# Kernel optimization log

Measured on AMD Instinct MI355X. Metric: run time of the kernel, lower is better.

The kernel has to match this reference:

```python
import jax, jax.numpy as jnp
import numpy as np

EPS = 1e-5
N_HEAD = 12
N_LAYER = 12
D = 768
VOCAB = 50257
SEQ = 1024


def layer_norm(x, w, b):
    m = jnp.mean(x, axis=-1, keepdims=True)
    v = jnp.mean(jnp.square(x - m), axis=-1, keepdims=True)
    return (x - m) * jax.lax.rsqrt(v + EPS) * w + b


def setup_inputs() -> dict:
    key = jax.random.key(0)
    ks = jax.random.split(key, 8)
    s = 0.02  # gpt2 init scale
    return {
        "input_ids": jax.random.randint(ks[0], (SEQ,), 0, VOCAB, dtype=jnp.int64 if jax.config.jax_enable_x64 else jnp.int32),
        "wte": jax.random.normal(ks[1], (VOCAB, D), jnp.float32) * s,
        "wpe": jax.random.normal(ks[2], (SEQ, D), jnp.float32) * s,
        "ln1_w": jnp.ones((N_LAYER, D), jnp.float32),
        "ln1_b": jnp.zeros((N_LAYER, D), jnp.float32),
        "qkv_w": jax.random.normal(ks[3], (N_LAYER, D, 3 * D), jnp.float32) * s,
        "qkv_b": jnp.zeros((N_LAYER, 3 * D), jnp.float32),
        "out_w": jax.random.normal(ks[4], (N_LAYER, D, D), jnp.float32) * s,
        "out_b": jnp.zeros((N_LAYER, D), jnp.float32),
        "ln2_w": jnp.ones((N_LAYER, D), jnp.float32),
        "ln2_b": jnp.zeros((N_LAYER, D), jnp.float32),
        "up_w": jax.random.normal(ks[5], (N_LAYER, D, 4 * D), jnp.float32) * s,
        "up_b": jnp.zeros((N_LAYER, 4 * D), jnp.float32),
        "down_w": jax.random.normal(ks[6], (N_LAYER, 4 * D, D), jnp.float32) * s,
        "down_b": jnp.zeros((N_LAYER, D), jnp.float32),
        "lnf_w": jnp.ones((D,), jnp.float32),
        "lnf_b": jnp.zeros((D,), jnp.float32),
    }


def _attention(x, qkv_w, qkv_b, out_w, out_b, causal_mask):
    S = x.shape[0]
    d = D // N_HEAD
    qkv = x @ qkv_w + qkv_b                  # [S, 3D]
    q, k, v = jnp.split(qkv, 3, axis=-1)     # each [S, D]
    q = q.reshape(S, N_HEAD, d)
    k = k.reshape(S, N_HEAD, d)
    v = v.reshape(S, N_HEAD, d)
    scores = jnp.einsum('shd,thd->hst', q, k) / np.sqrt(d).astype(np.float32)
    scores = jnp.where(causal_mask, scores, jnp.finfo(scores.dtype).min)
    p = jax.nn.softmax(scores, axis=-1)      # [H, S, S]
    o = jnp.einsum('hst,thd->shd', p, v).reshape(S, D)
    return o @ out_w + out_b


def reference(input_ids, wte, wpe, ln1_w, ln1_b, qkv_w, qkv_b, out_w, out_b,
              ln2_w, ln2_b, up_w, up_b, down_w, down_b, lnf_w, lnf_b):
    S = input_ids.shape[0]
    h0 = wte[input_ids] + wpe[jnp.arange(S)]        # [S, D]
    causal_mask = jnp.tril(jnp.ones((S, S), bool))

    layer_params = (ln1_w, ln1_b, qkv_w, qkv_b, out_w, out_b,
                    ln2_w, ln2_b, up_w, up_b, down_w, down_b)

    def step(x, p):
        l1w, l1b, qw, qb, ow, ob, l2w, l2b, uw, ub, dw, db = p
        x = x + _attention(layer_norm(x, l1w, l1b), qw, qb, ow, ob, causal_mask)
        x = x + (jax.nn.gelu(layer_norm(x, l2w, l2b) @ uw + ub, approximate=True) @ dw + db)
        return x, x

    h, ys = jax.lax.scan(step, h0, layer_params)
    layers_output = jnp.concatenate([h0[None], ys], axis=0)   # [L+1, S, D]
    return layer_norm(h, lnf_w, lnf_b), layers_output
```

## Files before the change

kernel.cpp:

```cpp
#include <hip/hip_runtime.h>

typedef __bf16 bf16_t;
typedef __bf16 bf16x8 __attribute__((ext_vector_type(8)));
typedef __bf16 bf16x4 __attribute__((ext_vector_type(4)));
typedef float f32x4 __attribute__((ext_vector_type(4)));

#define MFMA16(a, b, c) __builtin_amdgcn_mfma_f32_16x16x32_bf16(a, b, c, 0, 0, 0)

__device__ __forceinline__ f32x4 zero4() {
    f32x4 z = {0.f, 0.f, 0.f, 0.f};
    return z;
}

__device__ __forceinline__ float gelu_f(float v) {
    float u = 0.7978845608028654f * (v + 0.044715f * v * v * v);
    float e = __expf(2.0f * u);
    float th = 1.0f - 2.0f / (e + 1.0f);
    return 0.5f * v * (1.0f + th);
}

__device__ __forceinline__ void gload16(const bf16_t* g, bf16_t* l) {
    __builtin_amdgcn_global_load_lds((const __attribute__((address_space(1))) void*)g,
                                     (__attribute__((address_space(3))) void*)l, 16, 0, 0);
}

__global__ __launch_bounds__(256) void embed_kernel(const int* __restrict__ ids,
                                                    const float* __restrict__ wte,
                                                    const float* __restrict__ wpe,
                                                    float* __restrict__ x,
                                                    float* __restrict__ out0) {
    const int s = blockIdx.x;
    const int id = ids[s];
    const size_t base = (size_t)s * 768;
#pragma unroll
    for (int r = 0; r < 3; ++r) {
        int d = threadIdx.x + r * 256;
        float v = wte[(size_t)id * 768 + d] + wpe[base + d];
        x[base + d] = v;
        out0[base + d] = v;
    }
}

template <bool BF16OUT>
__global__ __launch_bounds__(256) void ln_kernel(const float* __restrict__ x,
                                                 const float* __restrict__ w,
                                                 const float* __restrict__ b,
                                                 void* __restrict__ outp) {
    const int row = blockIdx.x;
    const int t = threadIdx.x;
    const float* xr = x + (size_t)row * 768;
    float v0 = xr[t], v1 = xr[t + 256], v2 = xr[t + 512];
    float s = v0 + v1 + v2;
    float q = v0 * v0 + v1 * v1 + v2 * v2;
#pragma unroll
    for (int off = 32; off >= 1; off >>= 1) {
        s += __shfl_xor(s, off);
        q += __shfl_xor(q, off);
    }
    __shared__ float sh_s[4], sh_q[4];
    if ((t & 63) == 0) {
        sh_s[t >> 6] = s;
        sh_q[t >> 6] = q;
    }
    __syncthreads();
    s = sh_s[0] + sh_s[1] + sh_s[2] + sh_s[3];
    q = sh_q[0] + sh_q[1] + sh_q[2] + sh_q[3];
    const float mean = s * (1.0f / 768.0f);
    const float var = q * (1.0f / 768.0f) - mean * mean;
    const float rstd = rsqrtf(var + 1e-5f);
    float vv[3] = {v0, v1, v2};
#pragma unroll
    for (int r = 0; r < 3; ++r) {
        int d = t + r * 256;
        float y = (vv[r] - mean) * rstd * w[d] + b[d];
        if (BF16OUT)
            ((bf16_t*)outp)[(size_t)row * 768 + d] = (bf16_t)y;
        else
            ((float*)outp)[(size_t)row * 768 + d] = y;
    }
}

template <bool FINAL>
__global__ __launch_bounds__(256) void ln_reduce(const float* __restrict__ p0,
                                                 const float* __restrict__ p1,
                                                 const float* __restrict__ db,
                                                 float* __restrict__ x,
                                                 float* __restrict__ slice,
                                                 void* __restrict__ lnout,
                                                 const float* __restrict__ w,
                                                 const float* __restrict__ b) {
    const int row = blockIdx.x;
    const int t = threadIdx.x;
    const size_t base = (size_t)row * 768;
    float vv[3];
#pragma unroll
    for (int r = 0; r < 3; ++r) {
        int d = t + r * 256;
        float v = x[base + d] + p0[base + d] + p1[base + d] + db[d];
        vv[r] = v;
        x[base + d] = v;
        slice[base + d] = v;
    }
    float s = vv[0] + vv[1] + vv[2];
    float q = vv[0] * vv[0] + vv[1] * vv[1] + vv[2] * vv[2];
#pragma unroll
    for (int off = 32; off >= 1; off >>= 1) {
        s += __shfl_xor(s, off);
        q += __shfl_xor(q, off);
    }
    __shared__ float sh_s[4], sh_q[4];
    if ((t & 63) == 0) {
        sh_s[t >> 6] = s;
        sh_q[t >> 6] = q;
    }
    __syncthreads();
    s = sh_s[0] + sh_s[1] + sh_s[2] + sh_s[3];
    q = sh_q[0] + sh_q[1] + sh_q[2] + sh_q[3];
    const float mean = s * (1.0f / 768.0f);
    const float var = q * (1.0f / 768.0f) - mean * mean;
    const float rstd = rsqrtf(var + 1e-5f);
#pragma unroll
    for (int r = 0; r < 3; ++r) {
        int d = t + r * 256;
        float y = (vv[r] - mean) * rstd * w[d] + b[d];
        if (FINAL)
            ((float*)lnout)[base + d] = y;
        else
            ((bf16_t*)lnout)[base + d] = (bf16_t)y;
    }
}

__global__ __launch_bounds__(256) void transpose_cvt(const float* __restrict__ src0,
                                                     bf16_t* __restrict__ dst0, int K, int N) {
    const int l = blockIdx.z;
    const float* src = src0 + (size_t)l * K * N;
    bf16_t* dst = dst0 + (size_t)l * N * K;
    const int n0 = blockIdx.x * 32;
    const int k0 = blockIdx.y * 32;
    __shared__ float tile[32][36];
    const int t = threadIdx.x;
    const int r = t >> 3, c4 = (t & 7) * 4;
    const float4 v = *(const float4*)&src[(size_t)(k0 + r) * N + n0 + c4];
    tile[r][c4 + 0] = v.x;
    tile[r][c4 + 1] = v.y;
    tile[r][c4 + 2] = v.z;
    tile[r][c4 + 3] = v.w;
    __syncthreads();
    bf16x4 o;
    o[0] = (bf16_t)tile[c4 + 0][r];
    o[1] = (bf16_t)tile[c4 + 1][r];
    o[2] = (bf16_t)tile[c4 + 2][r];
    o[3] = (bf16_t)tile[c4 + 3][r];
    *(bf16x4*)&dst[(size_t)(n0 + r) * K + k0 + c4] = o;
}

template <int BM, int BN, bool GELU, bool RES>
__global__ __launch_bounds__(256) void gemm3(const bf16_t* __restrict__ A,
                                             const bf16_t* __restrict__ BT,
                                             const float* __restrict__ bias,
                                             const float* __restrict__ res,
                                             float* __restrict__ outF,
                                             bf16_t* __restrict__ outB, int N, int LDK,
                                             int KLEN) {
    constexpr int MW = BM / 32, NW = BN / 32;
    constexpr int TILE = (BM + BN) * 64;
    __shared__ __align__(16) bf16_t lds[2 * TILE];
    const int tid = threadIdx.x;
    const int lane = tid & 63, wv = tid >> 6, wm = wv >> 1, wn = wv & 1;
    const int lr = lane & 15, lg = lane >> 4;
    const int m0 = blockIdx.x * BM, n0 = blockIdx.y * BN;
    const bf16_t* Ap = A + (size_t)m0 * LDK + (size_t)blockIdx.z * KLEN;
    const bf16_t* Bp = BT + (size_t)n0 * LDK + (size_t)blockIdx.z * KLEN;

    f32x4 acc[MW][NW];
#pragma unroll
    for (int i = 0; i < MW; ++i)
#pragma unroll
        for (int j = 0; j < NW; ++j) acc[i][j] = zero4();

    const int KT = KLEN >> 6;

    auto stage = [&](int buf, int kt) {
        bf16_t* Ad = lds + buf * TILE;
        bf16_t* Bd = Ad + BM * 64;
#pragma unroll
        for (int i = 0; i < BM / 32; ++i) {
            int v = i * 256 + tid;
            int row = v >> 3, cg = v & 7;
            gload16(Ap + (size_t)row * LDK + kt * 64 + ((cg ^ (row & 7)) << 3), Ad + v * 8);
        }
#pragma unroll
        for (int i = 0; i < BN / 32; ++i) {
            int v = i * 256 + tid;
            int row = v >> 3, cg = v & 7;
            gload16(Bp + (size_t)row * LDK + kt * 64 + ((cg ^ (row & 7)) << 3), Bd + v * 8);
        }
    };

    stage(0, 0);
    int buf = 0;
    for (int kt = 0; kt < KT; ++kt) {
        __syncthreads();
        if (kt + 1 < KT) stage(buf ^ 1, kt + 1);
        const bf16_t* Ab = lds + buf * TILE;
        const bf16_t* Bb = Ab + BM * 64;
#pragma unroll
        for (int c = 0; c < 2; ++c) {
            bf16x8 af[MW], bfr[NW];
#pragma unroll
            for (int i = 0; i < MW; ++i) {
                int row = wm * (BM / 2) + i * 16 + lr;
                af[i] = *(const bf16x8*)&Ab[row * 64 + ((c * 32 + lg * 8) ^ ((row & 7) << 3))];
            }
#pragma unroll
            for (int j = 0; j < NW; ++j) {
                int row = wn * (BN / 2) + j * 16 + lr;
                bfr[j] = *(const bf16x8*)&Bb[row * 64 + ((c * 32 + lg * 8) ^ ((row & 7) << 3))];
            }
#pragma unroll
            for (int i = 0; i < MW; ++i)
#pragma unroll
                for (int j = 0; j < NW; ++j) acc[i][j] = MFMA16(af[i], bfr[j], acc[i][j]);
        }
        buf ^= 1;
    }

    float* o1 = outF ? outF + (size_t)blockIdx.z * ((size_t)1024 * N) : nullptr;
#pragma unroll
    for (int i = 0; i < MW; ++i) {
#pragma unroll
        for (int j = 0; j < NW; ++j) {
            const int col = n0 + wn * (BN / 2) + j * 16 + lr;
            const float bc = bias ? bias[col] : 0.f;
#pragma unroll
            for (int ii = 0; ii < 4; ++ii) {
                const int rrow = m0 + wm * (BM / 2) + i * 16 + lg * 4 + ii;
                float v = acc[i][j][ii] + bc;
                if (GELU) v = gelu_f(v);
                if (RES) v += res[(size_t)rrow * N + col];
                if (o1) o1[(size_t)rrow * N + col] = v;
                if (outB) outB[(size_t)rrow * N + col] = (bf16_t)v;
            }
        }
    }
}

__global__ __launch_bounds__(256) void attn_kernel(const bf16_t* __restrict__ qkv,
                                                   bf16_t* __restrict__ out) {
    const int qb = blockIdx.x;
    const int h = blockIdx.y;
    const int tid = threadIdx.x;
    const int w = tid >> 6, lane = tid & 63;
    const int lr = lane & 15, lg = lane >> 4;
    const int q0 = qb * 64;
    const int qr0 = q0 + w * 16;

    __shared__ bf16_t Ks[64][72];
    __shared__ bf16_t Vs[64][72];
    __shared__ bf16_t Ps[4][16][72];

    bf16x8 aq[2];
    {
        const size_t qoff = (size_t)(qr0 + lr) * 2304 + h * 64;
#pragma unroll
        for (int dt = 0; dt < 2; ++dt) {
            bf16x8 v = *(const bf16x8*)&qkv[qoff + dt * 32 + lg * 8];
#pragma unroll
            for (int i = 0; i < 8; ++i) v[i] = (bf16_t)((float)v[i] * 0.125f);
            aq[dt] = v;
        }
    }

    f32x4 oacc[4];
#pragma unroll
    for (int i = 0; i < 4; ++i) oacc[i] = zero4();
    float mrun[4], lrun[4];
#pragma unroll
    for (int i = 0; i < 4; ++i) {
        mrun[i] = -3.0e38f;
        lrun[i] = 0.f;
    }

    const int srow = tid >> 2, sseg = tid & 3;

    for (int kb = 0; kb <= qb; ++kb) {
        const int k0 = kb * 64;
        {
            const size_t roff = (size_t)(k0 + srow) * 2304 + h * 64 + sseg * 16;
            bf16x8 ka = *(const bf16x8*)&qkv[roff + 768];
            bf16x8 kbv = *(const bf16x8*)&qkv[roff + 768 + 8];
            bf16x8 va = *(const bf16x8*)&qkv[roff + 1536];
            bf16x8 vb = *(const bf16x8*)&qkv[roff + 1536 + 8];
            *(bf16x8*)&Ks[srow][sseg * 16] = ka;
            *(bf16x8*)&Ks[srow][sseg * 16 + 8] = kbv;
#pragma unroll
            for (int i = 0; i < 8; ++i) {
                Vs[sseg * 16 + i][srow] = va[i];
                Vs[sseg * 16 + 8 + i][srow] = vb[i];
            }
        }
        __syncthreads();

        f32x4 sacc[4];
#pragma unroll
        for (int i = 0; i < 4; ++i) sacc[i] = zero4();
#pragma unroll
        for (int kt = 0; kt < 4; ++kt)
#pragma unroll
            for (int dt = 0; dt < 2; ++dt) {
                bf16x8 bk = *(const bf16x8*)&Ks[kt * 16 + lr][dt * 32 + lg * 8];
                sacc[kt] = MFMA16(aq[dt], bk, sacc[kt]);
            }

        if (kb == qb) {
#pragma unroll
            for (int kt = 0; kt < 4; ++kt)
#pragma unroll
                for (int i = 0; i < 4; ++i)
                    if (k0 + kt * 16 + lr > qr0 + lg * 4 + i) sacc[kt][i] = -3.0e38f;
        }

#pragma unroll
        for (int i = 0; i < 4; ++i) {
            float rmax = fmaxf(fmaxf(sacc[0][i], sacc[1][i]), fmaxf(sacc[2][i], sacc[3][i]));
            rmax = fmaxf(rmax, __shfl_xor(rmax, 1));
            rmax = fmaxf(rmax, __shfl_xor(rmax, 2));
            rmax = fmaxf(rmax, __shfl_xor(rmax, 4));
            rmax = fmaxf(rmax, __shfl_xor(rmax, 8));
            const float mnew = fmaxf(mrun[i], rmax);
            const float sf = __expf(mrun[i] - mnew);
            mrun[i] = mnew;
            float rsum = 0.f;
#pragma unroll
            for (int kt = 0; kt < 4; ++kt) {
                float p = __expf(sacc[kt][i] - mnew);
                rsum += p;
                Ps[w][lg * 4 + i][kt * 16 + lr] = (bf16_t)p;
            }
            rsum += __shfl_xor(rsum, 1);
            rsum += __shfl_xor(rsum, 2);
            rsum += __shfl_xor(rsum, 4);
            rsum += __shfl_xor(rsum, 8);
            lrun[i] = lrun[i] * sf + rsum;
#pragma unroll
            for (int ot = 0; ot < 4; ++ot) oacc[ot][i] *= sf;
        }

        bf16x8 pa0 = *(const bf16x8*)&Ps[w][lr][lg * 8];
        bf16x8 pa1 = *(const bf16x8*)&Ps[w][lr][32 + lg * 8];
#pragma unroll
        for (int ot = 0; ot < 4; ++ot) {
            bf16x8 bv0 = *(const bf16x8*)&Vs[ot * 16 + lr][lg * 8];
            bf16x8 bv1 = *(const bf16x8*)&Vs[ot * 16 + lr][32 + lg * 8];
            oacc[ot] = MFMA16(pa0, bv0, oacc[ot]);
            oacc[ot] = MFMA16(pa1, bv1, oacc[ot]);
        }
        __syncthreads();
    }

#pragma unroll
    for (int ot = 0; ot < 4; ++ot)
#pragma unroll
        for (int i = 0; i < 4; ++i) {
            const int row = qr0 + lg * 4 + i;
            const float v = oacc[ot][i] / lrun[i];
            out[(size_t)row * 768 + h * 64 + ot * 16 + lr] = (bf16_t)v;
        }
}

extern "C" void kernel_launch(void* const* d_in, const int* in_sizes, int n_in, void* d_out,
                              int out_size, void* d_ws, size_t ws_size, hipStream_t stream) {
    const int* ids = (const int*)d_in[0];
    const float* wte = (const float*)d_in[1];
    const float* wpe = (const float*)d_in[2];
    const float* ln1_w = (const float*)d_in[3];
    const float* ln1_b = (const float*)d_in[4];
    const float* qkv_w = (const float*)d_in[5];
    const float* qkv_b = (const float*)d_in[6];
    const float* out_w = (const float*)d_in[7];
    const float* out_b = (const float*)d_in[8];
    const float* ln2_w = (const float*)d_in[9];
    const float* ln2_b = (const float*)d_in[10];
    const float* up_w = (const float*)d_in[11];
    const float* up_b = (const float*)d_in[12];
    const float* down_w = (const float*)d_in[13];
    const float* down_b = (const float*)d_in[14];
    const float* lnf_w = (const float*)d_in[15];
    const float* lnf_b = (const float*)d_in[16];

    char* ws = (char*)d_ws;
    float* x = (float*)(ws + 0);
    bf16_t* a_bf = (bf16_t*)(ws + 3145728);
    bf16_t* qkv_bf = (bf16_t*)(ws + 4718592);
    bf16_t* attn_bf = (bf16_t*)(ws + 9437184);
    bf16_t* u_bf = (bf16_t*)(ws + 11010048);
    float* p0 = (float*)(ws + 4718592);
    float* p1 = (float*)(ws + 7864320);
    bf16_t* wqkv_t = (bf16_t*)(ws + 17301504);
    bf16_t* wout_t = (bf16_t*)(ws + 59768832);
    bf16_t* wup_t = (bf16_t*)(ws + 73924608);
    bf16_t* wdown_t = (bf16_t*)(ws + 130547712);

    float* outF = (float*)d_out;
    const size_t SD = (size_t)1024 * 768;
    float* out_layers = outF + SD;

    transpose_cvt<<<dim3(72, 24, 12), 256, 0, stream>>>(qkv_w, wqkv_t, 768, 2304);
    transpose_cvt<<<dim3(24, 24, 12), 256, 0, stream>>>(out_w, wout_t, 768, 768);
    transpose_cvt<<<dim3(96, 24, 12), 256, 0, stream>>>(up_w, wup_t, 768, 3072);
    transpose_cvt<<<dim3(24, 96, 12), 256, 0, stream>>>(down_w, wdown_t, 3072, 768);

    embed_kernel<<<1024, 256, 0, stream>>>(ids, wte, wpe, x, out_layers);

    for (int l = 0; l < 12; ++l) {
        const size_t l768 = (size_t)l * 768;
        if (l == 0)
            ln_kernel<true><<<1024, 256, 0, stream>>>(x, ln1_w, ln1_b, a_bf);
        else
            ln_reduce<false><<<1024, 256, 0, stream>>>(p0, p1, down_b + (l - 1) * 768, x,
                                                       out_layers + (size_t)l * SD, a_bf,
                                                       ln1_w + l768, ln1_b + l768);
        gemm3<64, 64, false, false><<<dim3(16, 36), 256, 0, stream>>>(
            a_bf, wqkv_t + (size_t)l * 2304 * 768, qkv_b + (size_t)l * 2304, nullptr, nullptr,
            qkv_bf, 2304, 768, 768);
        attn_kernel<<<dim3(16, 12), 256, 0, stream>>>(qkv_bf, attn_bf);
        gemm3<32, 64, false, true><<<dim3(32, 12), 256, 0, stream>>>(
            attn_bf, wout_t + (size_t)l * 768 * 768, out_b + l768, x, x, nullptr, 768, 768,
            768);
        ln_kernel<true><<<1024, 256, 0, stream>>>(x, ln2_w + l768, ln2_b + l768, a_bf);
        gemm3<64, 64, true, false><<<dim3(16, 48), 256, 0, stream>>>(
            a_bf, wup_t + (size_t)l * 3072 * 768, up_b + (size_t)l * 3072, nullptr, nullptr,
            u_bf, 3072, 768, 768);
        gemm3<32, 64, false, false><<<dim3(32, 12, 2), 256, 0, stream>>>(
            u_bf, wdown_t + (size_t)l * 768 * 3072, nullptr, nullptr, p0, nullptr, 768, 3072,
            1536);
    }
    ln_reduce<true><<<1024, 256, 0, stream>>>(p0, p1, down_b + 11 * 768, x,
                                              out_layers + 12 * SD, outF, lnf_w, lnf_b);
}
```

Baseline: 1.199 ms.

## Rewrite attention with 16-row query blocks, split-K waves, and pre-transposed V

The QKV GEMM epilogue now also writes a transposed copy of V into a scratch buffer that is later reused by the MLP. The new attention kernel runs 16-query blocks over 768 workgroups of two waves, scheduled longest-first. Each wave handles alternate key blocks, reads K and V straight from global memory with no LDS staging or block barriers, and keeps P in registers. The two waves' partial softmax states are merged through LDS at the end. GEMM K-tile counts also become compile-time template constants so the loop can be fully unrolled.

```diff
diff --git a/kernel.cpp b/kernel.cpp
--- a/kernel.cpp
+++ b/kernel.cpp
@@ -4,6 +4,7 @@
 typedef __bf16 bf16x8 __attribute__((ext_vector_type(8)));
 typedef __bf16 bf16x4 __attribute__((ext_vector_type(4)));
 typedef float f32x4 __attribute__((ext_vector_type(4)));
+typedef int i32x4 __attribute__((ext_vector_type(4)));
 
 #define MFMA16(a, b, c) __builtin_amdgcn_mfma_f32_16x16x32_bf16(a, b, c, 0, 0, 0)
 
@@ -22,6 +23,12 @@
 __device__ __forceinline__ void gload16(const bf16_t* g, bf16_t* l) {
     __builtin_amdgcn_global_load_lds((const __attribute__((address_space(1))) void*)g,
                                      (__attribute__((address_space(3))) void*)l, 16, 0, 0);
+}
+
+__device__ __forceinline__ unsigned pack2(float a, float b) {
+    unsigned short ua = __builtin_bit_cast(unsigned short, (bf16_t)a);
+    unsigned short ub = __builtin_bit_cast(unsigned short, (bf16_t)b);
+    return (unsigned)ua | ((unsigned)ub << 16);
 }
 
 __global__ __launch_bounds__(256) void embed_kernel(const int* __restrict__ ids,
@@ -154,14 +161,14 @@
     *(bf16x4*)&dst[(size_t)(n0 + r) * K + k0 + c4] = o;
 }
 
-template <int BM, int BN, bool GELU, bool RES>
+template <int BM, int BN, int KTILES, bool GELU, bool RES, bool VT>
 __global__ __launch_bounds__(256) void gemm3(const bf16_t* __restrict__ A,
                                              const bf16_t* __restrict__ BT,
                                              const float* __restrict__ bias,
                                              const float* __restrict__ res,
                                              float* __restrict__ outF,
-                                             bf16_t* __restrict__ outB, int N, int LDK,
-                                             int KLEN) {
+                                             bf16_t* __restrict__ outB,
+                                             bf16_t* __restrict__ vt, int N, int LDK) {
     constexpr int MW = BM / 32, NW = BN / 32;
     constexpr int TILE = (BM + BN) * 64;
     __shared__ __align__(16) bf16_t lds[2 * TILE];
@@ -169,16 +176,14 @@
     const int lane = tid & 63, wv = tid >> 6, wm = wv >> 1, wn = wv & 1;
     const int lr = lane & 15, lg = lane >> 4;
     const int m0 = blockIdx.x * BM, n0 = blockIdx.y * BN;
-    const bf16_t* Ap = A + (size_t)m0 * LDK + (size_t)blockIdx.z * KLEN;
-    const bf16_t* Bp = BT + (size_t)n0 * LDK + (size_t)blockIdx.z * KLEN;
+    const bf16_t* Ap = A + (size_t)m0 * LDK + (size_t)blockIdx.z * (KTILES * 64);
+    const bf16_t* Bp = BT + (size_t)n0 * LDK + (size_t)blockIdx.z * (KTILES * 64);
 
     f32x4 acc[MW][NW];
 #pragma unroll
     for (int i = 0; i < MW; ++i)
 #pragma unroll
         for (int j = 0; j < NW; ++j) acc[i][j] = zero4();
-
-    const int KT = KLEN >> 6;
 
     auto stage = [&](int buf, int kt) {
         bf16_t* Ad = lds + buf * TILE;
@@ -199,9 +204,10 @@
 
     stage(0, 0);
     int buf = 0;
-    for (int kt = 0; kt < KT; ++kt) {
+#pragma unroll
+    for (int kt = 0; kt < KTILES; ++kt) {
         __syncthreads();
-        if (kt + 1 < KT) stage(buf ^ 1, kt + 1);
+        if (kt + 1 < KTILES) stage(buf ^ 1, kt + 1);
         const bf16_t* Ab = lds + buf * TILE;
         const bf16_t* Bb = Ab + BM * 64;
 #pragma unroll
@@ -232,6 +238,7 @@
         for (int j = 0; j < NW; ++j) {
             const int col = n0 + wn * (BN / 2) + j * 16 + lr;
             const float bc = bias ? bias[col] : 0.f;
+            float vr[4];
 #pragma unroll
             for (int ii = 0; ii < 4; ++ii) {
                 const int rrow = m0 + wm * (BM / 2) + i * 16 + lg * 4 + ii;
@@ -240,67 +247,52 @@
                 if (RES) v += res[(size_t)rrow * N + col];
                 if (o1) o1[(size_t)rrow * N + col] = v;
                 if (outB) outB[(size_t)rrow * N + col] = (bf16_t)v;
-            }
-        }
-    }
-}
-
-__global__ __launch_bounds__(256) void attn_kernel(const bf16_t* __restrict__ qkv,
-                                                   bf16_t* __restrict__ out) {
-    const int qb = blockIdx.x;
+                vr[ii] = v;
+            }
+            if (VT && col >= 1536) {
+                const int rrow0 = m0 + wm * (BM / 2) + i * 16 + lg * 4;
+                bf16x4 o;
+#pragma unroll
+                for (int ii = 0; ii < 4; ++ii) o[ii] = (bf16_t)vr[ii];
+                *(bf16x4*)&vt[(size_t)(col - 1536) * 1024 + rrow0] = o;
+            }
+        }
+    }
+}
+
+__global__ __launch_bounds__(128) void attn2_kernel(const bf16_t* __restrict__ qkv,
+                                                    const bf16_t* __restrict__ vt,
+                                                    bf16_t* __restrict__ out) {
+    const int qb = 63 - blockIdx.x;
     const int h = blockIdx.y;
-    const int tid = threadIdx.x;
-    const int w = tid >> 6, lane = tid & 63;
+    const int w = threadIdx.x >> 6;
+    const int lane = threadIdx.x & 63;
     const int lr = lane & 15, lg = lane >> 4;
-    const int q0 = qb * 64;
-    const int qr0 = q0 + w * 16;
-
-    __shared__ bf16_t Ks[64][72];
-    __shared__ bf16_t Vs[64][72];
-    __shared__ bf16_t Ps[4][16][72];
-
-    bf16x8 aq[2];
+    const int q0 = qb * 16;
+    const int NT = (q0 >> 6) + 1;
+
+    __shared__ float Osh[16][64];
+    __shared__ float mlsh[2][2][16];
+
+    bf16x8 bq[2];
     {
-        const size_t qoff = (size_t)(qr0 + lr) * 2304 + h * 64;
+        const size_t qoff = (size_t)(q0 + lr) * 2304 + h * 64;
 #pragma unroll
         for (int dt = 0; dt < 2; ++dt) {
             bf16x8 v = *(const bf16x8*)&qkv[qoff + dt * 32 + lg * 8];
 #pragma unroll
             for (int i = 0; i < 8; ++i) v[i] = (bf16_t)((float)v[i] * 0.125f);
-            aq[dt] = v;
+            bq[dt] = v;
         }
     }
 
     f32x4 oacc[4];
 #pragma unroll
     for (int i = 0; i < 4; ++i) oacc[i] = zero4();
-    float mrun[4], lrun[4];
-#pragma unroll
-    for (int i = 0; i < 4; ++i) {
-        mrun[i] = -3.0e38f;
-        lrun[i] = 0.f;
-    }
-
-    const int srow = tid >> 2, sseg = tid & 3;
-
-    for (int kb = 0; kb <= qb; ++kb) {
+    float m = -3.0e38f, l = 0.f;
+
+    for (int kb = w; kb < NT; kb += 2) {
         const int k0 = kb * 64;
-        {
-            const size_t roff = (size_t)(k0 + srow) * 2304 + h * 64 + sseg * 16;
-            bf16x8 ka = *(const bf16x8*)&qkv[roff + 768];
-            bf16x8 kbv = *(const bf16x8*)&qkv[roff + 768 + 8];
-            bf16x8 va = *(const bf16x8*)&qkv[roff + 1536];
-            bf16x8 vb = *(const bf16x8*)&qkv[roff + 1536 + 8];
-            *(bf16x8*)&Ks[srow][sseg * 16] = ka;
-            *(bf16x8*)&Ks[srow][sseg * 16 + 8] = kbv;
-#pragma unroll
-            for (int i = 0; i < 8; ++i) {
-                Vs[sseg * 16 + i][srow] = va[i];
-                Vs[sseg * 16 + 8 + i][srow] = vb[i];
-            }
-        }
-        __syncthreads();
-
         f32x4 sacc[4];
 #pragma unroll
         for (int i = 0; i < 4; ++i) sacc[i] = zero4();
@@ -308,64 +300,104 @@
         for (int kt = 0; kt < 4; ++kt)
 #pragma unroll
             for (int dt = 0; dt < 2; ++dt) {
-                bf16x8 bk = *(const bf16x8*)&Ks[kt * 16 + lr][dt * 32 + lg * 8];
-                sacc[kt] = MFMA16(aq[dt], bk, sacc[kt]);
-            }
-
-        if (kb == qb) {
+                bf16x8 ak = *(const bf16x8*)&qkv[(size_t)(k0 + kt * 16 + lr) * 2304 + 768 +
+                                                 h * 64 + dt * 32 + lg * 8];
+                sacc[kt] = MFMA16(ak, bq[dt], sacc[kt]);
+            }
+        if (kb == NT - 1) {
 #pragma unroll
             for (int kt = 0; kt < 4; ++kt)
 #pragma unroll
-                for (int i = 0; i < 4; ++i)
-                    if (k0 + kt * 16 + lr > qr0 + lg * 4 + i) sacc[kt][i] = -3.0e38f;
-        }
-
-#pragma unroll
-        for (int i = 0; i < 4; ++i) {
-            float rmax = fmaxf(fmaxf(sacc[0][i], sacc[1][i]), fmaxf(sacc[2][i], sacc[3][i]));
-            rmax = fmaxf(rmax, __shfl_xor(rmax, 1));
-            rmax = fmaxf(rmax, __shfl_xor(rmax, 2));
-            rmax = fmaxf(rmax, __shfl_xor(rmax, 4));
-            rmax = fmaxf(rmax, __shfl_xor(rmax, 8));
-            const float mnew = fmaxf(mrun[i], rmax);
-            const float sf = __expf(mrun[i] - mnew);
-            mrun[i] = mnew;
-            float rsum = 0.f;
-#pragma unroll
-            for (int kt = 0; kt < 4; ++kt) {
-                float p = __expf(sacc[kt][i] - mnew);
-                rsum += p;
-                Ps[w][lg * 4 + i][kt * 16 + lr] = (bf16_t)p;
-            }
-            rsum += __shfl_xor(rsum, 1);
-            rsum += __shfl_xor(rsum, 2);
-            rsum += __shfl_xor(rsum, 4);
-            rsum += __shfl_xor(rsum, 8);
-            lrun[i] = lrun[i] * sf + rsum;
-#pragma unroll
-            for (int ot = 0; ot < 4; ++ot) oacc[ot][i] *= sf;
-        }
-
-        bf16x8 pa0 = *(const bf16x8*)&Ps[w][lr][lg * 8];
-        bf16x8 pa1 = *(const bf16x8*)&Ps[w][lr][32 + lg * 8];
-#pragma unroll
-        for (int ot = 0; ot < 4; ++ot) {
-            bf16x8 bv0 = *(const bf16x8*)&Vs[ot * 16 + lr][lg * 8];
-            bf16x8 bv1 = *(const bf16x8*)&Vs[ot * 16 + lr][32 + lg * 8];
-            oacc[ot] = MFMA16(pa0, bv0, oacc[ot]);
-            oacc[ot] = MFMA16(pa1, bv1, oacc[ot]);
-        }
-        __syncthreads();
-    }
-
-#pragma unroll
-    for (int ot = 0; ot < 4; ++ot)
-#pragma unroll
-        for (int i = 0; i < 4; ++i) {
-            const int row = qr0 + lg * 4 + i;
-            const float v = oacc[ot][i] / lrun[i];
-            out[(size_t)row * 768 + h * 64 + ot * 16 + lr] = (bf16_t)v;
-        }
+                for (int ii = 0; ii < 4; ++ii)
+                    if (k0 + kt * 16 + lg * 4 + ii > q0 + lr) sacc[kt][ii] = -3.0e38f;
+        }
+
+        float pmax = -3.0e38f;
+#pragma unroll
+        for (int kt = 0; kt < 4; ++kt)
+#pragma unroll
+            for (int ii = 0; ii < 4; ++ii) pmax = fmaxf(pmax, sacc[kt][ii]);
+        pmax = fmaxf(pmax, __shfl_xor(pmax, 16));
+        pmax = fmaxf(pmax, __shfl_xor(pmax, 32));
+        const float mnew = fmaxf(m, pmax);
+        const float sf = __expf(m - mnew);
+        m = mnew;
+        float p[4][4];
+        float ps = 0.f;
+#pragma unroll
+        for (int kt = 0; kt < 4; ++kt)
+#pragma unroll
+            for (int ii = 0; ii < 4; ++ii) {
+                p[kt][ii] = __expf(sacc[kt][ii] - mnew);
+                ps += p[kt][ii];
+            }
+        ps += __shfl_xor(ps, 16);
+        ps += __shfl_xor(ps, 32);
+        l = l * sf + ps;
+        float sfr[4];
+#pragma unroll
+        for (int ii = 0; ii < 4; ++ii) sfr[ii] = __shfl(sf, lg * 4 + ii);
+#pragma unroll
+        for (int ot = 0; ot < 4; ++ot)
+#pragma unroll
+            for (int ii = 0; ii < 4; ++ii) oacc[ot][ii] *= sfr[ii];
+
+#pragma unroll
+        for (int c = 0; c < 2; ++c) {
+            i32x4 wds;
+            wds[0] = pack2(p[2 * c][0], p[2 * c][1]);
+            wds[1] = pack2(p[2 * c][2], p[2 * c][3]);
+            wds[2] = pack2(p[2 * c + 1][0], p[2 * c + 1][1]);
+            wds[3] = pack2(p[2 * c + 1][2], p[2 * c + 1][3]);
+            bf16x8 pa = __builtin_bit_cast(bf16x8, wds);
+#pragma unroll
+            for (int ot = 0; ot < 4; ++ot) {
+                const size_t vb =
+                    (size_t)(h * 64 + ot * 16 + lr) * 1024 + k0 + c * 32 + lg * 4;
+                bf16x4 v0 = *(const bf16x4*)&vt[vb];
+                bf16x4 v1 = *(const bf16x4*)&vt[vb + 16];
+                bf16x8 bv;
+#pragma unroll
+                for (int jj = 0; jj < 4; ++jj) {
+                    bv[jj] = v0[jj];
+                    bv[4 + jj] = v1[jj];
+                }
+                oacc[ot] = MFMA16(pa, bv, oacc[ot]);
+            }
+        }
+    }
+
+    if (w == 1) {
+        if (lg == 0) {
+            mlsh[1][0][lr] = m;
+            mlsh[1][1][lr] = l;
+        }
+#pragma unroll
+        for (int ot = 0; ot < 4; ++ot)
+#pragma unroll
+            for (int ii = 0; ii < 4; ++ii) Osh[lg * 4 + ii][ot * 16 + lr] = oacc[ot][ii];
+    } else {
+        if (lg == 0) {
+            mlsh[0][0][lr] = m;
+            mlsh[0][1][lr] = l;
+        }
+    }
+    __syncthreads();
+    if (w == 0) {
+#pragma unroll
+        for (int ot = 0; ot < 4; ++ot)
+#pragma unroll
+            for (int ii = 0; ii < 4; ++ii) {
+                const int q = lg * 4 + ii;
+                const float m0 = mlsh[0][0][q], l0 = mlsh[0][1][q];
+                const float m1 = mlsh[1][0][q], l1 = mlsh[1][1][q];
+                const float mm = fmaxf(m0, m1);
+                const float fa = __expf(m0 - mm), fb = __expf(m1 - mm);
+                const float ll = l0 * fa + l1 * fb;
+                const float v = (oacc[ot][ii] * fa + Osh[q][ot * 16 + lr] * fb) / ll;
+                out[(size_t)(q0 + q) * 768 + h * 64 + ot * 16 + lr] = (bf16_t)v;
+            }
+    }
 }
 
 extern "C" void kernel_launch(void* const* d_in, const int* in_sizes, int n_in, void* d_out,
@@ -394,6 +426,7 @@
     bf16_t* qkv_bf = (bf16_t*)(ws + 4718592);
     bf16_t* attn_bf = (bf16_t*)(ws + 9437184);
     bf16_t* u_bf = (bf16_t*)(ws + 11010048);
+    bf16_t* vt = (bf16_t*)(ws + 11010048);
     float* p0 = (float*)(ws + 4718592);
     float* p1 = (float*)(ws + 7864320);
     bf16_t* wqkv_t = (bf16_t*)(ws + 17301504);
@@ -420,20 +453,20 @@
             ln_reduce<false><<<1024, 256, 0, stream>>>(p0, p1, down_b + (l - 1) * 768, x,
                                                        out_layers + (size_t)l * SD, a_bf,
                                                        ln1_w + l768, ln1_b + l768);
-        gemm3<64, 64, false, false><<<dim3(16, 36), 256, 0, stream>>>(
+        gemm3<64, 64, 12, false, false, true><<<dim3(16, 36), 256, 0, stream>>>(
             a_bf, wqkv_t + (size_t)l * 2304 * 768, qkv_b + (size_t)l * 2304, nullptr, nullptr,
-            qkv_bf, 2304, 768, 768);
-        attn_kernel<<<dim3(16, 12), 256, 0, stream>>>(qkv_bf, attn_bf);
-        gemm3<32, 64, false, true><<<dim3(32, 12), 256, 0, stream>>>(
-            attn_bf, wout_t + (size_t)l * 768 * 768, out_b + l768, x, x, nullptr, 768, 768,
+            qkv_bf, vt, 2304, 768);
+        attn2_kernel<<<dim3(64, 12), 128, 0, stream>>>(qkv_bf, vt, attn_bf);
+        gemm3<32, 64, 12, false, true, false><<<dim3(32, 12), 256, 0, stream>>>(
+            attn_bf, wout_t + (size_t)l * 768 * 768, out_b + l768, x, x, nullptr, nullptr, 768,
             768);
         ln_kernel<true><<<1024, 256, 0, stream>>>(x, ln2_w + l768, ln2_b + l768, a_bf);
-        gemm3<64, 64, true, false><<<dim3(16, 48), 256, 0, stream>>>(
+        gemm3<64, 64, 12, true, false, false><<<dim3(16, 48), 256, 0, stream>>>(
             a_bf, wup_t + (size_t)l * 3072 * 768, up_b + (size_t)l * 3072, nullptr, nullptr,
-            u_bf, 3072, 768, 768);
-        gemm3<32, 64, false, false><<<dim3(32, 12, 2), 256, 0, stream>>>(
-            u_bf, wdown_t + (size_t)l * 768 * 3072, nullptr, nullptr, p0, nullptr, 768, 3072,
-            1536);
+            u_bf, nullptr, 3072, 768);
+        gemm3<32, 64, 24, false, false, false><<<dim3(32, 12, 2), 256, 0, stream>>>(
+            u_bf, wdown_t + (size_t)l * 768 * 3072, nullptr, nullptr, p0, nullptr, nullptr, 768,
+            3072);
     }
     ln_reduce<true><<<1024, 256, 0, stream>>>(p0, p1, down_b + 11 * 768, x,
                                               out_layers + 12 * SD, outF, lnf_w, lnf_b);
```

Result: slower. 1.371 ms (+14.3%).

## Split attention KV loop across warp pairs and shrink query tiles

Applied to the files above, without the earlier changes.

The attention kernel now handles 32 query rows per block instead of 64, doubling the grid to 384 blocks. Each pair of warps splits the key blocks between them, even and odd, staging two K/V tiles per round, and the two partial softmax states are merged through shared memory at the end. Blocks are issued heaviest-first by reversing the query-block index. The aim is to fill more compute units and shorten the critical path of the long causal rows. The cost is redundant K/V loads across blocks, more shared memory, and a final merge step.

```diff
diff --git a/kernel.cpp b/kernel.cpp
--- a/kernel.cpp
+++ b/kernel.cpp
@@ -245,19 +245,23 @@
     }
 }
 
-__global__ __launch_bounds__(256) void attn_kernel(const bf16_t* __restrict__ qkv,
-                                                   bf16_t* __restrict__ out) {
-    const int qb = blockIdx.x;
+__global__ __launch_bounds__(256) void attn3_kernel(const bf16_t* __restrict__ qkv,
+                                                    bf16_t* __restrict__ out) {
+    const int qb = 31 - blockIdx.x;
     const int h = blockIdx.y;
     const int tid = threadIdx.x;
     const int w = tid >> 6, lane = tid & 63;
     const int lr = lane & 15, lg = lane >> 4;
-    const int q0 = qb * 64;
-    const int qr0 = q0 + w * 16;
-
-    __shared__ bf16_t Ks[64][72];
-    __shared__ bf16_t Vs[64][72];
+    const int qsub = w & 1, ks = w >> 1;
+    const int q0 = qb * 32;
+    const int qr0 = q0 + qsub * 16;
+    const int NT = (q0 >> 6) + 1;
+
+    __shared__ bf16_t Ksh[2][64][72];
+    __shared__ bf16_t Vsh[2][64][72];
     __shared__ bf16_t Ps[4][16][72];
+    __shared__ float Osh[2][16][64];
+    __shared__ float mlsh[2][2][16];
 
     bf16x8 aq[2];
     {
@@ -281,91 +285,122 @@
         lrun[i] = 0.f;
     }
 
-    const int srow = tid >> 2, sseg = tid & 3;
-
-    for (int kb = 0; kb <= qb; ++kb) {
-        const int k0 = kb * 64;
-        {
-            const size_t roff = (size_t)(k0 + srow) * 2304 + h * 64 + sseg * 16;
-            bf16x8 ka = *(const bf16x8*)&qkv[roff + 768];
-            bf16x8 kbv = *(const bf16x8*)&qkv[roff + 768 + 8];
-            bf16x8 va = *(const bf16x8*)&qkv[roff + 1536];
-            bf16x8 vb = *(const bf16x8*)&qkv[roff + 1536 + 8];
-            *(bf16x8*)&Ks[srow][sseg * 16] = ka;
-            *(bf16x8*)&Ks[srow][sseg * 16 + 8] = kbv;
-#pragma unroll
-            for (int i = 0; i < 8; ++i) {
-                Vs[sseg * 16 + i][srow] = va[i];
-                Vs[sseg * 16 + 8 + i][srow] = vb[i];
+    const int st = tid >> 7;
+    const int srow = (tid >> 1) & 63;
+    const int rounds = (NT + 1) >> 1;
+
+    for (int rr = 0; rr < rounds; ++rr) {
+        const int skb = 2 * rr + st;
+        if (skb < NT) {
+            const int k0s = skb * 64;
+#pragma unroll
+            for (int s2 = 0; s2 < 2; ++s2) {
+                const int dbase = (tid & 1) * 32 + s2 * 16;
+                const size_t roff = (size_t)(k0s + srow) * 2304 + h * 64 + dbase;
+                bf16x8 ka = *(const bf16x8*)&qkv[roff + 768];
+                bf16x8 kbv = *(const bf16x8*)&qkv[roff + 768 + 8];
+                bf16x8 va = *(const bf16x8*)&qkv[roff + 1536];
+                bf16x8 vb = *(const bf16x8*)&qkv[roff + 1536 + 8];
+                *(bf16x8*)&Ksh[st][srow][dbase] = ka;
+                *(bf16x8*)&Ksh[st][srow][dbase + 8] = kbv;
+#pragma unroll
+                for (int i = 0; i < 8; ++i) {
+                    Vsh[st][dbase + i][srow] = va[i];
+                    Vsh[st][dbase + 8 + i][srow] = vb[i];
+                }
             }
         }
         __syncthreads();
 
-        f32x4 sacc[4];
-#pragma unroll
-        for (int i = 0; i < 4; ++i) sacc[i] = zero4();
-#pragma unroll
-        for (int kt = 0; kt < 4; ++kt)
-#pragma unroll
-            for (int dt = 0; dt < 2; ++dt) {
-                bf16x8 bk = *(const bf16x8*)&Ks[kt * 16 + lr][dt * 32 + lg * 8];
-                sacc[kt] = MFMA16(aq[dt], bk, sacc[kt]);
-            }
-
-        if (kb == qb) {
+        const int kb = 2 * rr + ks;
+        if (kb < NT) {
+            const int k0 = kb * 64;
+            f32x4 sacc[4];
+#pragma unroll
+            for (int i = 0; i < 4; ++i) sacc[i] = zero4();
 #pragma unroll
             for (int kt = 0; kt < 4; ++kt)
 #pragma unroll
-                for (int i = 0; i < 4; ++i)
-                    if (k0 + kt * 16 + lr > qr0 + lg * 4 + i) sacc[kt][i] = -3.0e38f;
-        }
-
-#pragma unroll
-        for (int i = 0; i < 4; ++i) {
-            float rmax = fmaxf(fmaxf(sacc[0][i], sacc[1][i]), fmaxf(sacc[2][i], sacc[3][i]));
-            rmax = fmaxf(rmax, __shfl_xor(rmax, 1));
-            rmax = fmaxf(rmax, __shfl_xor(rmax, 2));
-            rmax = fmaxf(rmax, __shfl_xor(rmax, 4));
-            rmax = fmaxf(rmax, __shfl_xor(rmax, 8));
-            const float mnew = fmaxf(mrun[i], rmax);
-            const float sf = __expf(mrun[i] - mnew);
-            mrun[i] = mnew;
-            float rsum = 0.f;
-#pragma unroll
-            for (int kt = 0; kt < 4; ++kt) {
-                float p = __expf(sacc[kt][i] - mnew);
-                rsum += p;
-                Ps[w][lg * 4 + i][kt * 16 + lr] = (bf16_t)p;
-            }
-            rsum += __shfl_xor(rsum, 1);
-            rsum += __shfl_xor(rsum, 2);
-            rsum += __shfl_xor(rsum, 4);
-            rsum += __shfl_xor(rsum, 8);
-            lrun[i] = lrun[i] * sf + rsum;
-#pragma unroll
-            for (int ot = 0; ot < 4; ++ot) oacc[ot][i] *= sf;
-        }
-
-        bf16x8 pa0 = *(const bf16x8*)&Ps[w][lr][lg * 8];
-        bf16x8 pa1 = *(const bf16x8*)&Ps[w][lr][32 + lg * 8];
-#pragma unroll
-        for (int ot = 0; ot < 4; ++ot) {
-            bf16x8 bv0 = *(const bf16x8*)&Vs[ot * 16 + lr][lg * 8];
-            bf16x8 bv1 = *(const bf16x8*)&Vs[ot * 16 + lr][32 + lg * 8];
-            oacc[ot] = MFMA16(pa0, bv0, oacc[ot]);
-            oacc[ot] = MFMA16(pa1, bv1, oacc[ot]);
+                for (int dt = 0; dt < 2; ++dt) {
+                    bf16x8 bk = *(const bf16x8*)&Ksh[ks][kt * 16 + lr][dt * 32 + lg * 8];
+                    sacc[kt] = MFMA16(aq[dt], bk, sacc[kt]);
+                }
+
+            if (kb == NT - 1) {
+#pragma unroll
+                for (int kt = 0; kt < 4; ++kt)
+#pragma unroll
+                    for (int i = 0; i < 4; ++i)
+                        if (k0 + kt * 16 + lr > qr0 + lg * 4 + i) sacc[kt][i] = -3.0e38f;
+            }
+
+#pragma unroll
+            for (int i = 0; i < 4; ++i) {
+                float rmax = fmaxf(fmaxf(sacc[0][i], sacc[1][i]), fmaxf(sacc[2][i], sacc[3][i]));
+                rmax = fmaxf(rmax, __shfl_xor(rmax, 1));
+                rmax = fmaxf(rmax, __shfl_xor(rmax, 2));
+                rmax = fmaxf(rmax, __shfl_xor(rmax, 4));
+                rmax = fmaxf(rmax, __shfl_xor(rmax, 8));
+                const float mnew = fmaxf(mrun[i], rmax);
+                const float sf = __expf(mrun[i] - mnew);
+                mrun[i] = mnew;
+                float rsum = 0.f;
+#pragma unroll
+                for (int kt = 0; kt < 4; ++kt) {
+                    float p = __expf(sacc[kt][i] - mnew);
+                    rsum += p;
+                    Ps[w][lg * 4 + i][kt * 16 + lr] = (bf16_t)p;
+                }
+                rsum += __shfl_xor(rsum, 1);
+                rsum += __shfl_xor(rsum, 2);
+                rsum += __shfl_xor(rsum, 4);
+                rsum += __shfl_xor(rsum, 8);
+                lrun[i] = lrun[i] * sf + rsum;
+#pragma unroll
+                for (int ot = 0; ot < 4; ++ot) oacc[ot][i] *= sf;
+            }
+
+            bf16x8 pa0 = *(const bf16x8*)&Ps[w][lr][lg * 8];
+            bf16x8 pa1 = *(const bf16x8*)&Ps[w][lr][32 + lg * 8];
+#pragma unroll
+            for (int ot = 0; ot < 4; ++ot) {
+                bf16x8 bv0 = *(const bf16x8*)&Vsh[ks][ot * 16 + lr][lg * 8];
+                bf16x8 bv1 = *(const bf16x8*)&Vsh[ks][ot * 16 + lr][32 + lg * 8];
+                oacc[ot] = MFMA16(pa0, bv0, oacc[ot]);
+                oacc[ot] = MFMA16(pa1, bv1, oacc[ot]);
+            }
         }
         __syncthreads();
     }
 
-#pragma unroll
-    for (int ot = 0; ot < 4; ++ot)
-#pragma unroll
-        for (int i = 0; i < 4; ++i) {
-            const int row = qr0 + lg * 4 + i;
-            const float v = oacc[ot][i] / lrun[i];
-            out[(size_t)row * 768 + h * 64 + ot * 16 + lr] = (bf16_t)v;
-        }
+    if (ks == 1) {
+        if (lr == 0) {
+#pragma unroll
+            for (int i = 0; i < 4; ++i) {
+                mlsh[qsub][0][lg * 4 + i] = mrun[i];
+                mlsh[qsub][1][lg * 4 + i] = lrun[i];
+            }
+        }
+#pragma unroll
+        for (int ot = 0; ot < 4; ++ot)
+#pragma unroll
+            for (int i = 0; i < 4; ++i) Osh[qsub][lg * 4 + i][ot * 16 + lr] = oacc[ot][i];
+    }
+    __syncthreads();
+    if (ks == 0) {
+#pragma unroll
+        for (int ot = 0; ot < 4; ++ot)
+#pragma unroll
+            for (int i = 0; i < 4; ++i) {
+                const int row = lg * 4 + i;
+                const float m1 = mlsh[qsub][0][row], l1 = mlsh[qsub][1][row];
+                const float mm = fmaxf(mrun[i], m1);
+                const float fa = __expf(mrun[i] - mm), fb = __expf(m1 - mm);
+                const float ll = lrun[i] * fa + l1 * fb;
+                const float v = (oacc[ot][i] * fa + Osh[qsub][row][ot * 16 + lr] * fb) / ll;
+                out[(size_t)(qr0 + row) * 768 + h * 64 + ot * 16 + lr] = (bf16_t)v;
+            }
+    }
 }
 
 extern "C" void kernel_launch(void* const* d_in, const int* in_sizes, int n_in, void* d_out,
@@ -423,7 +458,7 @@
         gemm3<64, 64, false, false><<<dim3(16, 36), 256, 0, stream>>>(
             a_bf, wqkv_t + (size_t)l * 2304 * 768, qkv_b + (size_t)l * 2304, nullptr, nullptr,
             qkv_bf, 2304, 768, 768);
-        attn_kernel<<<dim3(16, 12), 256, 0, stream>>>(qkv_bf, attn_bf);
+        attn3_kernel<<<dim3(32, 12), 256, 0, stream>>>(qkv_bf, attn_bf);
         gemm3<32, 64, false, true><<<dim3(32, 12), 256, 0, stream>>>(
             attn_bf, wout_t + (size_t)l * 768 * 768, out_b + l768, x, x, nullptr, 768, 768,
             768);
```

New measurement: 1.149 ms. 4.2% less time.
